# Performance work log

Hardware: AMD Instinct MI355X
Metric: run time of the kernel (lower is better)

## Reference

```python
import jax, jax.numpy as jnp
import numpy as np

B, S, D, H = 8, 1024, 768, 12
DK = D // H  # 64


def setup_inputs() -> dict:
    key = jax.random.key(0)
    ks = jax.random.split(key, 11)
    scale = 1.0 / np.sqrt(D)
    inp = {
        "query": jax.random.normal(ks[0], (B, S, D), jnp.float32),
        "key": jax.random.normal(ks[1], (B, S, D), jnp.float32),
        "value": jax.random.normal(ks[2], (B, S, D), jnp.float32),
        "Wq": jax.random.normal(ks[3], (D, D), jnp.float32) * scale,
        "bq": jnp.zeros((D,), jnp.float32),
        "Wk": jax.random.normal(ks[4], (D, D), jnp.float32) * scale,
        "bk": jnp.zeros((D,), jnp.float32),
        "Wv": jax.random.normal(ks[5], (D, D), jnp.float32) * scale,
        "bv": jnp.zeros((D,), jnp.float32),
        "Wd": jax.random.normal(ks[6], (D, D), jnp.float32) * scale,
        "bd": jnp.zeros((D,), jnp.float32),
    }
    return inp


def reference(query, key, value, Wq, bq, Wk, bk, Wv, bv, Wd, bd):
    # QKV projections (torch Linear equivalent: x @ W + b with W stored [in,out])
    q = query @ Wq + bq  # [B,S,D]
    k = key @ Wk + bk
    v = value @ Wv + bv
    # split heads -> [B,H,S,DK]
    q = q.reshape(B, S, H, DK).transpose(0, 2, 1, 3)
    k = k.reshape(B, S, H, DK).transpose(0, 2, 1, 3)
    v = v.reshape(B, S, H, DK).transpose(0, 2, 1, 3)
    scores = jnp.einsum("bhqd,bhkd->bhqk", q, k) / jnp.sqrt(jnp.float32(DK))
    weights = jax.nn.softmax(scores, axis=-1)  # attn dropout = identity (eval)
    ctx = jnp.einsum("bhqk,bhkd->bhqd", weights, v)
    context = ctx.transpose(0, 2, 1, 3).reshape(B, S, D)
    hidden_states = context @ Wd + bd  # out dropout = identity (eval)
    return (hidden_states, context)
```

## Files before the change

kernel.cpp:

```cpp
#include <hip/hip_runtime.h>
#include <hip/hip_bf16.h>
#include <math.h>

constexpr int Bc = 8;
constexpr int Sc = 1024;
constexpr int Dc = 768;
constexpr int Hc = 12;
constexpr int DKc = 64;
constexpr int BSc = Bc * Sc;
constexpr size_t HEAD_ELEMS = (size_t)Bc * Hc * Sc * DKc;
constexpr size_t OUT_ELEMS  = (size_t)Bc * Sc * Dc;

typedef __attribute__((ext_vector_type(8))) short short8;
typedef __attribute__((ext_vector_type(4))) short short4v;
typedef __attribute__((ext_vector_type(4))) float f32x4;

__device__ __forceinline__ short f2bf(float x) {
  __hip_bfloat16 h = __float2bfloat16(x);
  short r;
  __builtin_memcpy(&r, &h, 2);
  return r;
}

__device__ __forceinline__ void gload16(const void* g, void* l) {
  __builtin_amdgcn_global_load_lds(
      (const __attribute__((address_space(1))) void*)g,
      (__attribute__((address_space(3))) void*)l, 16, 0, 0);
}

__global__ __launch_bounds__(256) void wtrans4(
    const float* __restrict__ W0, const float* __restrict__ W1,
    const float* __restrict__ W2, const float* __restrict__ W3,
    __hip_bfloat16* __restrict__ Wt0) {
  __shared__ float t[32][33];
  const int z = blockIdx.z;
  const float* W = (z == 0) ? W0 : (z == 1) ? W1 : (z == 2) ? W2 : W3;
  __hip_bfloat16* Wt = Wt0 + (size_t)z * Dc * Dc;
  const int tx = threadIdx.x & 31, ty = threadIdx.x >> 5;
  const int bx = blockIdx.x * 32;
  const int by = blockIdx.y * 32;
  #pragma unroll
  for (int i = 0; i < 32; i += 8)
    t[ty + i][tx] = W[(size_t)(by + ty + i) * Dc + bx + tx];
  __syncthreads();
  #pragma unroll
  for (int i = 0; i < 32; i += 8)
    Wt[(size_t)(bx + ty + i) * Dc + by + tx] = __float2bfloat16(t[tx][ty + i]);
}

__global__ __launch_bounds__(256) void gemm_qkv(
    const float* __restrict__ Aq, const float* __restrict__ Ak,
    const float* __restrict__ Av, const __hip_bfloat16* __restrict__ Wt0,
    const float* __restrict__ bq, const float* __restrict__ bk,
    const float* __restrict__ bv, __hip_bfloat16* __restrict__ out0) {
  __shared__ __hip_bfloat16 As[128 * 64];
  __shared__ __hip_bfloat16 Bs[128 * 64];

  const int tid = threadIdx.x;
  const int lane = tid & 63;
  const int wv = tid >> 6;
  const int l15 = lane & 15;
  const int g = lane >> 4;
  const int wr = wv >> 1, wc = wv & 1;

  const int proj = blockIdx.y;
  const float* A = (proj == 0) ? Aq : (proj == 1) ? Ak : Av;
  const float* bias = (proj == 0) ? bq : (proj == 1) ? bk : bv;
  const __hip_bfloat16* Wt = Wt0 + (size_t)proj * Dc * Dc;
  __hip_bfloat16* out = out0 + (size_t)proj * HEAD_ELEMS;

  const int orig = blockIdx.x;
  const int swz = (orig & 7) * 48 + (orig >> 3);
  const int rb = swz / (Dc / 128);
  const int cb = swz % (Dc / 128);
  const int row0 = rb * 128, col0 = cb * 128;

  f32x4 acc[4][4];
  #pragma unroll
  for (int ai = 0; ai < 4; ai++)
    #pragma unroll
    for (int bj = 0; bj < 4; bj++) acc[ai][bj] = f32x4{0.f, 0.f, 0.f, 0.f};

  for (int k0 = 0; k0 < Dc; k0 += 64) {
    __syncthreads();

    #pragma unroll
    for (int j = 0; j < 4; j++) {
      const int r = j * 32 + wv * 8 + (lane >> 3);
      const __hip_bfloat16* gp =
          Wt + (size_t)(col0 + r) * Dc + k0 + (lane & 7) * 8;
      gload16(gp, &Bs[(j * 32 + wv * 8) * 64]);
    }

    #pragma unroll
    for (int i = 0; i < 4; i++) {
      const int id = tid + i * 256;
      const int r = id >> 3, gi = id & 7;
      const float* ap = A + (size_t)(row0 + r) * Dc + k0 + gi * 8;
      const float4 f0 = *reinterpret_cast<const float4*>(ap);
      const float4 f1 = *reinterpret_cast<const float4*>(ap + 4);
      short8 s;
      s[0] = f2bf(f0.x); s[1] = f2bf(f0.y); s[2] = f2bf(f0.z); s[3] = f2bf(f0.w);
      s[4] = f2bf(f1.x); s[5] = f2bf(f1.y); s[6] = f2bf(f1.z); s[7] = f2bf(f1.w);
      *reinterpret_cast<short8*>(&As[r * 64 + gi * 8]) = s;
    }
    __syncthreads();

    #pragma unroll
    for (int kk = 0; kk < 2; kk++) {
      short8 a[4], b[4];
      #pragma unroll
      for (int ai = 0; ai < 4; ai++)
        a[ai] = *reinterpret_cast<const short8*>(
            &As[(wr * 64 + ai * 16 + l15) * 64 + kk * 32 + g * 8]);
      #pragma unroll
      for (int bj = 0; bj < 4; bj++)
        b[bj] = *reinterpret_cast<const short8*>(
            &Bs[(wc * 64 + bj * 16 + l15) * 64 + kk * 32 + g * 8]);
      #pragma unroll
      for (int ai = 0; ai < 4; ai++)
        #pragma unroll
        for (int bj = 0; bj < 4; bj++)
          acc[ai][bj] = __builtin_amdgcn_mfma_f32_16x16x32_bf16(
              a[ai], b[bj], acc[ai][bj], 0, 0, 0);
    }
  }

  const int mb = row0 + wr * 64, nb = col0 + wc * 64;
  if (proj < 2) {
    #pragma unroll
    for (int ai = 0; ai < 4; ai++)
      #pragma unroll
      for (int bj = 0; bj < 4; bj++) {
        const int n = nb + bj * 16 + l15;
        const int h_ = n >> 6, dk = n & 63;
        const float bn = bias[n];
        #pragma unroll
        for (int reg = 0; reg < 4; reg++) {
          const int m = mb + ai * 16 + g * 4 + reg;
          const int b_ = m >> 10, s_ = m & 1023;
          out[(((size_t)(b_ * Hc + h_)) * Sc + s_) * DKc + dk] =
              __float2bfloat16(acc[ai][bj][reg] + bn);
        }
      }
  } else {
    #pragma unroll
    for (int ai = 0; ai < 4; ai++)
      #pragma unroll
      for (int bj = 0; bj < 4; bj++) {
        const int n = nb + bj * 16 + l15;
        const int h_ = n >> 6, dk = n & 63;
        const float bn = bias[n];
        const int m0 = mb + ai * 16 + g * 4;
        const int b_ = m0 >> 10, s0 = m0 & 1023;
        short4v sv;
        sv[0] = f2bf(acc[ai][bj][0] + bn);
        sv[1] = f2bf(acc[ai][bj][1] + bn);
        sv[2] = f2bf(acc[ai][bj][2] + bn);
        sv[3] = f2bf(acc[ai][bj][3] + bn);
        *reinterpret_cast<short4v*>(
            &out[(((size_t)(b_ * Hc + h_)) * DKc + dk) * Sc + s0]) = sv;
      }
  }
}

__global__ __launch_bounds__(256) void gemm_out(
    const float* __restrict__ A, const __hip_bfloat16* __restrict__ Wt,
    const float* __restrict__ bias, float* __restrict__ out) {
  __shared__ __hip_bfloat16 As[128 * 64];
  __shared__ __hip_bfloat16 Bs[64 * 64];

  const int tid = threadIdx.x;
  const int lane = tid & 63;
  const int wv = tid >> 6;
  const int l15 = lane & 15;
  const int g = lane >> 4;
  const int wr = wv >> 1, wc = wv & 1;

  const int orig = blockIdx.x;
  const int swz = (orig & 7) * 96 + (orig >> 3);
  const int rb = swz / (Dc / 64);
  const int cb = swz % (Dc / 64);
  const int row0 = rb * 128, col0 = cb * 64;

  f32x4 acc[4][2];
  #pragma unroll
  for (int ai = 0; ai < 4; ai++)
    #pragma unroll
    for (int bj = 0; bj < 2; bj++) acc[ai][bj] = f32x4{0.f, 0.f, 0.f, 0.f};

  for (int k0 = 0; k0 < Dc; k0 += 64) {
    __syncthreads();

    #pragma unroll
    for (int j = 0; j < 2; j++) {
      const int r = j * 32 + wv * 8 + (lane >> 3);
      const __hip_bfloat16* gp =
          Wt + (size_t)(col0 + r) * Dc + k0 + (lane & 7) * 8;
      gload16(gp, &Bs[(j * 32 + wv * 8) * 64]);
    }

    #pragma unroll
    for (int i = 0; i < 4; i++) {
      const int id = tid + i * 256;
      const int r = id >> 3, gi = id & 7;
      const float* ap = A + (size_t)(row0 + r) * Dc + k0 + gi * 8;
      const float4 f0 = *reinterpret_cast<const float4*>(ap);
      const float4 f1 = *reinterpret_cast<const float4*>(ap + 4);
      short8 s;
      s[0] = f2bf(f0.x); s[1] = f2bf(f0.y); s[2] = f2bf(f0.z); s[3] = f2bf(f0.w);
      s[4] = f2bf(f1.x); s[5] = f2bf(f1.y); s[6] = f2bf(f1.z); s[7] = f2bf(f1.w);
      *reinterpret_cast<short8*>(&As[r * 64 + gi * 8]) = s;
    }
    __syncthreads();

    #pragma unroll
    for (int kk = 0; kk < 2; kk++) {
      short8 a[4], b[2];
      #pragma unroll
      for (int ai = 0; ai < 4; ai++)
        a[ai] = *reinterpret_cast<const short8*>(
            &As[(wr * 64 + ai * 16 + l15) * 64 + kk * 32 + g * 8]);
      #pragma unroll
      for (int bj = 0; bj < 2; bj++)
        b[bj] = *reinterpret_cast<const short8*>(
            &Bs[(wc * 32 + bj * 16 + l15) * 64 + kk * 32 + g * 8]);
      #pragma unroll
      for (int ai = 0; ai < 4; ai++)
        #pragma unroll
        for (int bj = 0; bj < 2; bj++)
          acc[ai][bj] = __builtin_amdgcn_mfma_f32_16x16x32_bf16(
              a[ai], b[bj], acc[ai][bj], 0, 0, 0);
    }
  }

  const int mb = row0 + wr * 64, nb = col0 + wc * 32;
  #pragma unroll
  for (int ai = 0; ai < 4; ai++)
    #pragma unroll
    for (int bj = 0; bj < 2; bj++) {
      const int n = nb + bj * 16 + l15;
      const float bn = bias[n];
      #pragma unroll
      for (int reg = 0; reg < 4; reg++) {
        const int m = mb + ai * 16 + g * 4 + reg;
        out[(size_t)m * Dc + n] = acc[ai][bj][reg] + bn;
      }
    }
}

__global__ __launch_bounds__(256) void attn_mfma(
    const __hip_bfloat16* __restrict__ Q, const __hip_bfloat16* __restrict__ K,
    const __hip_bfloat16* __restrict__ Vt, float* __restrict__ ctx) {
  __shared__ __hip_bfloat16 Ks[64 * 64];
  __shared__ __hip_bfloat16 Vs[64 * 64];

  const int tid = threadIdx.x;
  const int lane = tid & 63;
  const int w = tid >> 6;
  const int l15 = lane & 15;
  const int g = lane >> 4;

  const int cpx = gridDim.x >> 3;
  const int bid = blockIdx.x;
  const int wid = (bid & 7) * cpx + (bid >> 3);
  const int bh = wid >> 4;
  const int qt = wid & 15;
  const int qbase = qt * 64 + w * 16;

  const __hip_bfloat16* Qb = Q + (size_t)bh * Sc * DKc;
  const __hip_bfloat16* Kb = K + (size_t)bh * Sc * DKc;
  const __hip_bfloat16* Vtb = Vt + (size_t)bh * DKc * Sc;

  short8 qf[2];
  {
    const __hip_bfloat16* qp = Qb + (size_t)(qbase + l15) * DKc + g * 8;
    qf[0] = *reinterpret_cast<const short8*>(qp);
    qf[1] = *reinterpret_cast<const short8*>(qp + 32);
  }

  f32x4 Oacc[4];
  #pragma unroll
  for (int dt = 0; dt < 4; dt++) Oacc[dt] = f32x4{0.f, 0.f, 0.f, 0.f};
  float m_run = -1e30f, l_run = 0.f;

  constexpr float SM_SCALE = 0.125f * 1.44269504088896340736f;

  for (int kt = 0; kt < Sc; kt += 64) {
    __syncthreads();
    #pragma unroll
    for (int it = 0; it < 2; it++) {
      const int tt = tid + it * 256;
      const int row = tt >> 3, s = tt & 7;
      const float4 kv = *reinterpret_cast<const float4*>(
          Kb + (size_t)(kt + row) * DKc + s * 8);
      const float4 vv = *reinterpret_cast<const float4*>(
          Vtb + (size_t)row * Sc + kt + s * 8);
      const int off = row * 128 + ((s ^ (row & 7)) << 4);
      *reinterpret_cast<float4*>((char*)Ks + off) = kv;
      *reinterpret_cast<float4*>((char*)Vs + off) = vv;
    }
    __syncthreads();

    f32x4 sacc[4];
    #pragma unroll
    for (int mt = 0; mt < 4; mt++) sacc[mt] = f32x4{0.f, 0.f, 0.f, 0.f};
    #pragma unroll
    for (int c = 0; c < 2; c++) {
      #pragma unroll
      for (int mt = 0; mt < 4; mt++) {
        const int row = mt * 16 + l15;
        const short8 kf = *reinterpret_cast<const short8*>(
            (char*)Ks + row * 128 + (((g + 4 * c) ^ (row & 7)) << 4));
        sacc[mt] =
            __builtin_amdgcn_mfma_f32_16x16x32_bf16(kf, qf[c], sacc[mt], 0, 0, 0);
      }
    }

    float tmax = -1e30f;
    #pragma unroll
    for (int s = 0; s < 4; s++)
      #pragma unroll
      for (int r = 0; r < 4; r++) tmax = fmaxf(tmax, sacc[s][r]);
    tmax = fmaxf(tmax, __shfl_xor(tmax, 16));
    tmax = fmaxf(tmax, __shfl_xor(tmax, 32));
    const float mnew = fmaxf(m_run, tmax);
    const float alpha = __builtin_amdgcn_exp2f((m_run - mnew) * SM_SCALE);
    m_run = mnew;
    float wgt[4][4];
    float wsum = 0.f;
    #pragma unroll
    for (int s = 0; s < 4; s++)
      #pragma unroll
      for (int r = 0; r < 4; r++) {
        wgt[s][r] = __builtin_amdgcn_exp2f((sacc[s][r] - mnew) * SM_SCALE);
        wsum += wgt[s][r];
      }
    l_run = l_run * alpha + wsum;

    float ar[4];
    #pragma unroll
    for (int r = 0; r < 4; r++) ar[r] = __shfl(alpha, g * 4 + r);
    #pragma unroll
    for (int dt = 0; dt < 4; dt++)
      #pragma unroll
      for (int r = 0; r < 4; r++) Oacc[dt][r] *= ar[r];

    short8 pa[2];
    #pragma unroll
    for (int c = 0; c < 2; c++)
      #pragma unroll
      for (int i = 0; i < 8; i++) pa[c][i] = f2bf(wgt[2 * c + (i >> 2)][i & 3]);

    #pragma unroll
    for (int dt = 0; dt < 4; dt++) {
      const int row = dt * 16 + l15;
      const int rb2 = row * 128;
      const int sw = row & 7;
      const int gl = (g & 1) * 8;
      const int gh = g >> 1;
      #pragma unroll
      for (int c = 0; c < 2; c++) {
        const short4v v0 = *reinterpret_cast<const short4v*>(
            (char*)Vs + rb2 + ((((4 * c + 0) + gh) ^ sw) << 4) + gl);
        const short4v v1 = *reinterpret_cast<const short4v*>(
            (char*)Vs + rb2 + ((((4 * c + 2) + gh) ^ sw) << 4) + gl);
        const short8 vf =
            __builtin_shufflevector(v0, v1, 0, 1, 2, 3, 4, 5, 6, 7);
        Oacc[dt] =
            __builtin_amdgcn_mfma_f32_16x16x32_bf16(pa[c], vf, Oacc[dt], 0, 0, 0);
      }
    }
  }

  l_run += __shfl_xor(l_run, 16);
  l_run += __shfl_xor(l_run, 32);
  float linv[4];
  #pragma unroll
  for (int r = 0; r < 4; r++) linv[r] = 1.0f / __shfl(l_run, g * 4 + r);

  const int b_ = bh / Hc, h_ = bh % Hc;
  #pragma unroll
  for (int dt = 0; dt < 4; dt++)
    #pragma unroll
    for (int r = 0; r < 4; r++) {
      const int qa = qbase + g * 4 + r;
      float* p = ctx + ((size_t)(b_ * Sc + qa)) * Dc + h_ * 64 + dt * 16 + l15;
      *p = Oacc[dt][r] * linv[r];
    }
}

extern "C" void kernel_launch(void* const* d_in, const int* in_sizes, int n_in,
                              void* d_out, int out_size, void* d_ws,
                              size_t ws_size, hipStream_t stream) {
  const float* query = (const float*)d_in[0];
  const float* key_  = (const float*)d_in[1];
  const float* value = (const float*)d_in[2];
  const float* Wq = (const float*)d_in[3];
  const float* bq = (const float*)d_in[4];
  const float* Wk = (const float*)d_in[5];
  const float* bk = (const float*)d_in[6];
  const float* Wv = (const float*)d_in[7];
  const float* bv = (const float*)d_in[8];
  const float* Wd = (const float*)d_in[9];
  const float* bd = (const float*)d_in[10];

  float* out = (float*)d_out;
  float* hidden = out;
  float* context = out + OUT_ELEMS;

  __hip_bfloat16* Qw  = (__hip_bfloat16*)d_ws;
  __hip_bfloat16* Kw  = Qw + HEAD_ELEMS;
  __hip_bfloat16* Vtw = Kw + HEAD_ELEMS;
  __hip_bfloat16* WtQ = Vtw + HEAD_ELEMS;
  __hip_bfloat16* WtD = WtQ + 3 * (size_t)Dc * Dc;

  wtrans4<<<dim3(Dc / 32, Dc / 32, 4), 256, 0, stream>>>(Wq, Wk, Wv, Wd, WtQ);

  gemm_qkv<<<dim3((BSc / 128) * (Dc / 128), 3), 256, 0, stream>>>(
      query, key_, value, WtQ, bq, bk, bv, Qw);

  attn_mfma<<<Bc * Hc * (Sc / 64), 256, 0, stream>>>(Qw, Kw, Vtw, context);

  gemm_out<<<(BSc / 128) * (Dc / 64), 256, 0, stream>>>(
      context, WtD, bd, hidden);
}
```

Before: 289.4 us.

## Pre-cast activations to bf16 and double-buffer GEMMs with direct LDS loads

```diff
diff --git a/kernel.cpp b/kernel.cpp
--- a/kernel.cpp
+++ b/kernel.cpp
@@ -26,6 +26,22 @@
   __builtin_amdgcn_global_load_lds(
       (const __attribute__((address_space(1))) void*)g,
       (__attribute__((address_space(3))) void*)l, 16, 0, 0);
+}
+
+__global__ __launch_bounds__(256) void cast3(
+    const float* __restrict__ q, const float* __restrict__ k,
+    const float* __restrict__ v, __hip_bfloat16* __restrict__ dq,
+    __hip_bfloat16* __restrict__ dk, __hip_bfloat16* __restrict__ dv) {
+  const int which = blockIdx.y;
+  const float* src = (which == 0) ? q : (which == 1) ? k : v;
+  __hip_bfloat16* dst = (which == 0) ? dq : (which == 1) ? dk : dv;
+  const size_t i = ((size_t)blockIdx.x * 256 + threadIdx.x) * 8;
+  const float4 f0 = *reinterpret_cast<const float4*>(src + i);
+  const float4 f1 = *reinterpret_cast<const float4*>(src + i + 4);
+  short8 s;
+  s[0] = f2bf(f0.x); s[1] = f2bf(f0.y); s[2] = f2bf(f0.z); s[3] = f2bf(f0.w);
+  s[4] = f2bf(f1.x); s[5] = f2bf(f1.y); s[6] = f2bf(f1.z); s[7] = f2bf(f1.w);
+  *reinterpret_cast<short8*>(dst + i) = s;
 }
 
 __global__ __launch_bounds__(256) void wtrans4(
@@ -48,13 +64,59 @@
     Wt[(size_t)(bx + ty + i) * Dc + by + tx] = __float2bfloat16(t[tx][ty + i]);
 }
 
+__device__ __forceinline__ void stage_tiles(
+    const __hip_bfloat16* A, const __hip_bfloat16* Wt, int row0, int col0,
+    int k0, int wv, int lane, __hip_bfloat16* bufA, __hip_bfloat16* bufB) {
+  #pragma unroll
+  for (int j = 0; j < 2; j++) {
+    const int rr = j * 64 + wv * 16;
+    const int r = rr + (lane >> 2);
+    const int kc = k0 + (lane & 3) * 8;
+    gload16(A + (size_t)(row0 + r) * Dc + kc, bufA + rr * 32);
+    gload16(Wt + (size_t)(col0 + r) * Dc + kc, bufB + rr * 32);
+  }
+}
+
+__device__ __forceinline__ void compute_tiles(
+    const __hip_bfloat16* bufA, const __hip_bfloat16* bufB, int wr, int wc,
+    int l15, int g, f32x4 (&acc)[4][4]) {
+  short8 a[4], b[4];
+  #pragma unroll
+  for (int ai = 0; ai < 4; ai++)
+    a[ai] = *reinterpret_cast<const short8*>(
+        &bufA[(wr * 64 + ai * 16 + l15) * 32 + g * 8]);
+  #pragma unroll
+  for (int bj = 0; bj < 4; bj++)
+    b[bj] = *reinterpret_cast<const short8*>(
+        &bufB[(wc * 64 + bj * 16 + l15) * 32 + g * 8]);
+  #pragma unroll
+  for (int ai = 0; ai < 4; ai++)
+    #pragma unroll
+    for (int bj = 0; bj < 4; bj++)
+      acc[ai][bj] = __builtin_amdgcn_mfma_f32_16x16x32_bf16(
+          a[ai], b[bj], acc[ai][bj], 0, 0, 0);
+}
+
+#define GEMM_PIPELINE(A_, Wt_)                                          \
+  stage_tiles(A_, Wt_, row0, col0, 0, wv, lane, As0, Bs0);              \
+  __syncthreads();                                                      \
+  for (int t = 0; t < 24; t += 2) {                                     \
+    stage_tiles(A_, Wt_, row0, col0, (t + 1) * 32, wv, lane, As1, Bs1); \
+    compute_tiles(As0, Bs0, wr, wc, l15, g, acc);                       \
+    __syncthreads();                                                    \
+    if (t + 2 < 24)                                                     \
+      stage_tiles(A_, Wt_, row0, col0, (t + 2) * 32, wv, lane, As0, Bs0);\
+    compute_tiles(As1, Bs1, wr, wc, l15, g, acc);                       \
+    __syncthreads();                                                    \
+  }
+
 __global__ __launch_bounds__(256) void gemm_qkv(
-    const float* __restrict__ Aq, const float* __restrict__ Ak,
-    const float* __restrict__ Av, const __hip_bfloat16* __restrict__ Wt0,
+    const __hip_bfloat16* __restrict__ Aq, const __hip_bfloat16* __restrict__ Ak,
+    const __hip_bfloat16* __restrict__ Av, const __hip_bfloat16* __restrict__ Wt0,
     const float* __restrict__ bq, const float* __restrict__ bk,
     const float* __restrict__ bv, __hip_bfloat16* __restrict__ out0) {
-  __shared__ __hip_bfloat16 As[128 * 64];
-  __shared__ __hip_bfloat16 Bs[128 * 64];
+  __shared__ __hip_bfloat16 As0[128 * 32], Bs0[128 * 32];
+  __shared__ __hip_bfloat16 As1[128 * 32], Bs1[128 * 32];
 
   const int tid = threadIdx.x;
   const int lane = tid & 63;
@@ -64,16 +126,15 @@
   const int wr = wv >> 1, wc = wv & 1;
 
   const int proj = blockIdx.y;
-  const float* A = (proj == 0) ? Aq : (proj == 1) ? Ak : Av;
+  const __hip_bfloat16* A = (proj == 0) ? Aq : (proj == 1) ? Ak : Av;
   const float* bias = (proj == 0) ? bq : (proj == 1) ? bk : bv;
   const __hip_bfloat16* Wt = Wt0 + (size_t)proj * Dc * Dc;
   __hip_bfloat16* out = out0 + (size_t)proj * HEAD_ELEMS;
 
   const int orig = blockIdx.x;
   const int swz = (orig & 7) * 48 + (orig >> 3);
-  const int rb = swz / (Dc / 128);
-  const int cb = swz % (Dc / 128);
-  const int row0 = rb * 128, col0 = cb * 128;
+  const int row0 = (swz / (Dc / 128)) * 128;
+  const int col0 = (swz % (Dc / 128)) * 128;
 
   f32x4 acc[4][4];
   #pragma unroll
@@ -81,50 +142,7 @@
     #pragma unroll
     for (int bj = 0; bj < 4; bj++) acc[ai][bj] = f32x4{0.f, 0.f, 0.f, 0.f};
 
-  for (int k0 = 0; k0 < Dc; k0 += 64) {
-    __syncthreads();
-
-    #pragma unroll
-    for (int j = 0; j < 4; j++) {
-      const int r = j * 32 + wv * 8 + (lane >> 3);
-      const __hip_bfloat16* gp =
-          Wt + (size_t)(col0 + r) * Dc + k0 + (lane & 7) * 8;
-      gload16(gp, &Bs[(j * 32 + wv * 8) * 64]);
-    }
-
-    #pragma unroll
-    for (int i = 0; i < 4; i++) {
-      const int id = tid + i * 256;
-      const int r = id >> 3, gi = id & 7;
-      const float* ap = A + (size_t)(row0 + r) * Dc + k0 + gi * 8;
-      const float4 f0 = *reinterpret_cast<const float4*>(ap);
-      const float4 f1 = *reinterpret_cast<const float4*>(ap + 4);
-      short8 s;
-      s[0] = f2bf(f0.x); s[1] = f2bf(f0.y); s[2] = f2bf(f0.z); s[3] = f2bf(f0.w);
-      s[4] = f2bf(f1.x); s[5] = f2bf(f1.y); s[6] = f2bf(f1.z); s[7] = f2bf(f1.w);
-      *reinterpret_cast<short8*>(&As[r * 64 + gi * 8]) = s;
-    }
-    __syncthreads();
-
-    #pragma unroll
-    for (int kk = 0; kk < 2; kk++) {
-      short8 a[4], b[4];
-      #pragma unroll
-      for (int ai = 0; ai < 4; ai++)
-        a[ai] = *reinterpret_cast<const short8*>(
-            &As[(wr * 64 + ai * 16 + l15) * 64 + kk * 32 + g * 8]);
-      #pragma unroll
-      for (int bj = 0; bj < 4; bj++)
-        b[bj] = *reinterpret_cast<const short8*>(
-            &Bs[(wc * 64 + bj * 16 + l15) * 64 + kk * 32 + g * 8]);
-      #pragma unroll
-      for (int ai = 0; ai < 4; ai++)
-        #pragma unroll
-        for (int bj = 0; bj < 4; bj++)
-          acc[ai][bj] = __builtin_amdgcn_mfma_f32_16x16x32_bf16(
-              a[ai], b[bj], acc[ai][bj], 0, 0, 0);
-    }
-  }
+  GEMM_PIPELINE(A, Wt)
 
   const int mb = row0 + wr * 64, nb = col0 + wc * 64;
   if (proj < 2) {
@@ -164,11 +182,11 @@
   }
 }
 
-__global__ __launch_bounds__(256) void gemm_out(
-    const float* __restrict__ A, const __hip_bfloat16* __restrict__ Wt,
+__global__ __launch_bounds__(256) void gemm_o(
+    const __hip_bfloat16* __restrict__ A, const __hip_bfloat16* __restrict__ Wt,
     const float* __restrict__ bias, float* __restrict__ out) {
-  __shared__ __hip_bfloat16 As[128 * 64];
-  __shared__ __hip_bfloat16 Bs[64 * 64];
+  __shared__ __hip_bfloat16 As0[128 * 32], Bs0[128 * 32];
+  __shared__ __hip_bfloat16 As1[128 * 32], Bs1[128 * 32];
 
   const int tid = threadIdx.x;
   const int lane = tid & 63;
@@ -178,67 +196,23 @@
   const int wr = wv >> 1, wc = wv & 1;
 
   const int orig = blockIdx.x;
-  const int swz = (orig & 7) * 96 + (orig >> 3);
-  const int rb = swz / (Dc / 64);
-  const int cb = swz % (Dc / 64);
-  const int row0 = rb * 128, col0 = cb * 64;
-
-  f32x4 acc[4][2];
+  const int swz = (orig & 7) * 48 + (orig >> 3);
+  const int row0 = (swz / (Dc / 128)) * 128;
+  const int col0 = (swz % (Dc / 128)) * 128;
+
+  f32x4 acc[4][4];
   #pragma unroll
   for (int ai = 0; ai < 4; ai++)
     #pragma unroll
-    for (int bj = 0; bj < 2; bj++) acc[ai][bj] = f32x4{0.f, 0.f, 0.f, 0.f};
-
-  for (int k0 = 0; k0 < Dc; k0 += 64) {
-    __syncthreads();
-
-    #pragma unroll
-    for (int j = 0; j < 2; j++) {
-      const int r = j * 32 + wv * 8 + (lane >> 3);
-      const __hip_bfloat16* gp =
-          Wt + (size_t)(col0 + r) * Dc + k0 + (lane & 7) * 8;
-      gload16(gp, &Bs[(j * 32 + wv * 8) * 64]);
-    }
-
-    #pragma unroll
-    for (int i = 0; i < 4; i++) {
-      const int id = tid + i * 256;
-      const int r = id >> 3, gi = id & 7;
-      const float* ap = A + (size_t)(row0 + r) * Dc + k0 + gi * 8;
-      const float4 f0 = *reinterpret_cast<const float4*>(ap);
-      const float4 f1 = *reinterpret_cast<const float4*>(ap + 4);
-      short8 s;
-      s[0] = f2bf(f0.x); s[1] = f2bf(f0.y); s[2] = f2bf(f0.z); s[3] = f2bf(f0.w);
-      s[4] = f2bf(f1.x); s[5] = f2bf(f1.y); s[6] = f2bf(f1.z); s[7] = f2bf(f1.w);
-      *reinterpret_cast<short8*>(&As[r * 64 + gi * 8]) = s;
-    }
-    __syncthreads();
-
-    #pragma unroll
-    for (int kk = 0; kk < 2; kk++) {
-      short8 a[4], b[2];
-      #pragma unroll
-      for (int ai = 0; ai < 4; ai++)
-        a[ai] = *reinterpret_cast<const short8*>(
-            &As[(wr * 64 + ai * 16 + l15) * 64 + kk * 32 + g * 8]);
-      #pragma unroll
-      for (int bj = 0; bj < 2; bj++)
-        b[bj] = *reinterpret_cast<const short8*>(
-            &Bs[(wc * 32 + bj * 16 + l15) * 64 + kk * 32 + g * 8]);
-      #pragma unroll
-      for (int ai = 0; ai < 4; ai++)
-        #pragma unroll
-        for (int bj = 0; bj < 2; bj++)
-          acc[ai][bj] = __builtin_amdgcn_mfma_f32_16x16x32_bf16(
-              a[ai], b[bj], acc[ai][bj], 0, 0, 0);
-    }
-  }
-
-  const int mb = row0 + wr * 64, nb = col0 + wc * 32;
+    for (int bj = 0; bj < 4; bj++) acc[ai][bj] = f32x4{0.f, 0.f, 0.f, 0.f};
+
+  GEMM_PIPELINE(A, Wt)
+
+  const int mb = row0 + wr * 64, nb = col0 + wc * 64;
   #pragma unroll
   for (int ai = 0; ai < 4; ai++)
     #pragma unroll
-    for (int bj = 0; bj < 2; bj++) {
+    for (int bj = 0; bj < 4; bj++) {
       const int n = nb + bj * 16 + l15;
       const float bn = bias[n];
       #pragma unroll
@@ -251,7 +225,8 @@
 
 __global__ __launch_bounds__(256) void attn_mfma(
     const __hip_bfloat16* __restrict__ Q, const __hip_bfloat16* __restrict__ K,
-    const __hip_bfloat16* __restrict__ Vt, float* __restrict__ ctx) {
+    const __hip_bfloat16* __restrict__ Vt, float* __restrict__ ctx,
+    __hip_bfloat16* __restrict__ ctxb) {
   __shared__ __hip_bfloat16 Ks[64 * 64];
   __shared__ __hip_bfloat16 Vs[64 * 64];
 
@@ -385,8 +360,11 @@
     #pragma unroll
     for (int r = 0; r < 4; r++) {
       const int qa = qbase + g * 4 + r;
-      float* p = ctx + ((size_t)(b_ * Sc + qa)) * Dc + h_ * 64 + dt * 16 + l15;
-      *p = Oacc[dt][r] * linv[r];
+      const size_t idx =
+          ((size_t)(b_ * Sc + qa)) * Dc + h_ * 64 + dt * 16 + l15;
+      const float val = Oacc[dt][r] * linv[r];
+      ctx[idx] = val;
+      ctxb[idx] = __float2bfloat16(val);
     }
 }
 
@@ -409,19 +387,26 @@
   float* hidden = out;
   float* context = out + OUT_ELEMS;
 
+  __hip_bfloat16* Aq = (__hip_bfloat16*)hidden;
+  __hip_bfloat16* Ak = Aq + OUT_ELEMS;
+
   __hip_bfloat16* Qw  = (__hip_bfloat16*)d_ws;
   __hip_bfloat16* Kw  = Qw + HEAD_ELEMS;
   __hip_bfloat16* Vtw = Kw + HEAD_ELEMS;
   __hip_bfloat16* WtQ = Vtw + HEAD_ELEMS;
   __hip_bfloat16* WtD = WtQ + 3 * (size_t)Dc * Dc;
+  __hip_bfloat16* Av  = WtQ + 4 * (size_t)Dc * Dc;
+  __hip_bfloat16* ctxb = Av;
 
   wtrans4<<<dim3(Dc / 32, Dc / 32, 4), 256, 0, stream>>>(Wq, Wk, Wv, Wd, WtQ);
+  cast3<<<dim3(OUT_ELEMS / 8 / 256, 3), 256, 0, stream>>>(
+      query, key_, value, Aq, Ak, Av);
 
   gemm_qkv<<<dim3((BSc / 128) * (Dc / 128), 3), 256, 0, stream>>>(
-      query, key_, value, WtQ, bq, bk, bv, Qw);
-
-  attn_mfma<<<Bc * Hc * (Sc / 64), 256, 0, stream>>>(Qw, Kw, Vtw, context);
-
-  gemm_out<<<(BSc / 128) * (Dc / 64), 256, 0, stream>>>(
-      context, WtD, bd, hidden);
-}
+      Aq, Ak, Av, WtQ, bq, bk, bv, Qw);
+
+  attn_mfma<<<Bc * Hc * (Sc / 64), 256, 0, stream>>>(Qw, Kw, Vtw, context,
+                                                     ctxb);
+
+  gemm_o<<<(BSc / 128) * (Dc / 128), 256, 0, stream>>>(ctxb, WtD, bd, hidden);
+}
```

Result: faster. 271.0 us (-6.4%).
